# Optimization experiments

Hardware: AMD Instinct MI355X
Metric: run time of the kernel (lower is better)

The kernel has to match this reference:

```python
import jax, jax.numpy as jnp
import numpy as np

D_MODEL = 768
BATCH = 4096
RANK_DIST = [(4, 512), (8, 256), (16, 128), (32, 64), (64, 32)]


@jax.custom_vjp
def jumprelu(x):
    # hard threshold at 0 in fwd; full straight-through estimator in bwd
    return x * (x > 0.0).astype(x.dtype)


def _jr_fwd(x):
    return jumprelu(x), None


def _jr_bwd(res, g):
    return (g,)


jumprelu.defvjp(_jr_fwd, _jr_bwd)


def setup_inputs() -> dict:
    key = jax.random.key(0)
    keys = jax.random.split(key, 1 + 3 * len(RANK_DIST))
    inp = {"x": jax.random.normal(keys[0], (BATCH, D_MODEL), dtype=jnp.float32)}
    for i, (n, r) in enumerate(RANK_DIST):
        kV, kU, kE = keys[1 + 3 * i], keys[2 + 3 * i], keys[3 + 3 * i]
        scale = (1.0 / (D_MODEL * r)) ** 0.25
        inp[f"V{i}"] = scale * jax.random.normal(kV, (n, r, D_MODEL), dtype=jnp.float32)
        inp[f"U{i}"] = scale * jax.random.normal(kU, (n, D_MODEL, r), dtype=jnp.float32)
        enc = jax.random.normal(kE, (n, D_MODEL), dtype=jnp.float32)
        inp[f"enc{i}"] = enc / jnp.linalg.norm(enc, axis=1, keepdims=True)
        inp[f"b{i}"] = jnp.full((n,), -1.0, dtype=jnp.float32)
    return inp


def _group_forward(x, V, U, enc, b):
    n, r, d = V.shape
    pre = x @ enc.T - b                      # (b, n)
    gate = jumprelu(pre)                     # (b, n)
    Vx = jnp.einsum("nrd,bd->nbr", V, x)    # (n, b, r)
    # fused: UVx gated by gate then summed over transforms n
    out = jnp.einsum("ndr,nbr,bn->bd", U, Vx, gate)  # (b, d)
    u_norms = jnp.linalg.norm(U.reshape(n, -1), axis=1)
    v_norms = jnp.linalg.norm(V.reshape(n, -1), axis=1)
    frob = u_norms * v_norms / jnp.sqrt(jnp.asarray(d * r, dtype=x.dtype))
    return out, gate, frob


def reference(x, V0, U0, enc0, b0, V1, U1, enc1, b1, V2, U2, enc2, b2,
              V3, U3, enc3, b3, V4, U4, enc4, b4):
    Vs = [V0, V1, V2, V3, V4]
    Us = [U0, U1, U2, U3, U4]
    encs = [enc0, enc1, enc2, enc3, enc4]
    bs = [b0, b1, b2, b3, b4]
    output = jnp.zeros_like(x)
    total_sparsity = jnp.asarray(0.0, dtype=x.dtype)
    total_active = jnp.asarray(0.0, dtype=x.dtype)
    gate_acts = []
    for V, U, enc, b in zip(Vs, Us, encs, bs):
        g_out, gate, frob = _group_forward(x, V, U, enc, b)
        output = output + g_out
        mean_abs_gate = jnp.abs(gate).mean(axis=0)
        total_sparsity = total_sparsity + (jnp.tanh(mean_abs_gate) * frob).sum()
        total_active = total_active + (gate > 0).astype(x.dtype).sum(axis=1).mean()
        gate_acts.append(gate)
    return (output, total_sparsity, total_active, *gate_acts)
```

## Files before the change

### kernel.cpp

```cpp
#include <hip/hip_runtime.h>

#define BATCH 4096
#define DM 768
#define LTOT 10240
#define NG 124

typedef __bf16 bf16x8 __attribute__((ext_vector_type(8)));
typedef short short8 __attribute__((ext_vector_type(8)));
typedef float f32x4 __attribute__((ext_vector_type(4)));

struct Ptr5 { const float* p[5]; };

__device__ __forceinline__ unsigned short f2bf(float f) {
    unsigned u = __builtin_bit_cast(unsigned, f);
    unsigned r = (u + 0x7FFFu + ((u >> 16) & 1u)) >> 16;
    return (unsigned short)r;
}

__device__ __forceinline__ short8 pack8(float4 a, float4 b) {
    union { unsigned short u[8]; short8 s; } o;
    o.u[0] = f2bf(a.x); o.u[1] = f2bf(a.y); o.u[2] = f2bf(a.z); o.u[3] = f2bf(a.w);
    o.u[4] = f2bf(b.x); o.u[5] = f2bf(b.y); o.u[6] = f2bf(b.z); o.u[7] = f2bf(b.w);
    return o.s;
}


__global__ __launch_bounds__(256) void prep_k(const float* __restrict__ x,
                                              Ptr5 vp, Ptr5 up, Ptr5 ep, Ptr5 bp,
                                              unsigned short* __restrict__ vb,
                                              unsigned short* __restrict__ w2t,
                                              unsigned short* __restrict__ xb,
                                              float* __restrict__ gate_ws,
                                              float* __restrict__ outg,
                                              float* __restrict__ vslot,
                                              float* __restrict__ uslot,
                                              float* __restrict__ gslot,
                                              float* __restrict__ aslot) {
    const int basen[5] = {0, 4, 12, 28, 60};
    int bx = blockIdx.x;
    int tid = threadIdx.x;
    if (bx < 32) {
        __shared__ unsigned short lA[128 * 64];
        __shared__ unsigned short lB[128 * 64];
        __shared__ float sgs[128];
        __shared__ float sac;
        int wave = tid >> 6, lane = tid & 63;
        int wm = wave >> 1, wn = wave & 1;
        int lan15 = lane & 15, quad = lane >> 4;
        int sw = lan15 & 7;
        int m0 = bx * 128;
        f32x4 acc[4][4] = {};
        for (int k0 = 0; k0 < DM; k0 += 64) {
            __syncthreads();
            #pragma unroll
            for (int i = 0; i < 4; i++) {
                int gidx = i * 256 + tid;
                int row = gidx >> 3, kb = gidx & 7;
                int r7 = row & 7;
                int la = (row >> 3) * 512 + r7 * 64 + (kb ^ r7) * 8;
                int sidx = (m0 + row) * 192 + (k0 >> 2) + kb * 2;
                float4 a0 = ((const float4*)x)[sidx];
                float4 a1 = ((const float4*)x)[sidx + 1];
                *(short8*)(lA + la) = pack8(a0, a1);
                float4 b0 = {0.f, 0.f, 0.f, 0.f}, b1 = {0.f, 0.f, 0.f, 0.f};
                if (row < NG) {
                    int g = (row < 4) ? 0 : (row < 12) ? 1 : (row < 28) ? 2 :
                            (row < 60) ? 3 : 4;
                    int ni = row - basen[g];
                    int eidx = ni * 192 + (k0 >> 2) + kb * 2;
                    b0 = ((const float4*)ep.p[g])[eidx];
                    b1 = ((const float4*)ep.p[g])[eidx + 1];
                }
                *(short8*)(lB + la) = pack8(b0, b1);
            }
            __syncthreads();
            #pragma unroll
            for (int kk = 0; kk < 2; kk++) {
                int kb = kk * 4 + quad;
                int kel = (kb ^ sw) * 8;
                bf16x8 af[4], bfr[4];
                #pragma unroll
                for (int t = 0; t < 4; t++) {
                    short8 ra = *(const short8*)(lA + (wm * 64 + t * 16 + lan15) * 64 + kel);
                    short8 rb = *(const short8*)(lB + (wn * 64 + t * 16 + lan15) * 64 + kel);
                    af[t]  = __builtin_bit_cast(bf16x8, ra);
                    bfr[t] = __builtin_bit_cast(bf16x8, rb);
                }
                #pragma unroll
                for (int mt = 0; mt < 4; mt++)
                    #pragma unroll
                    for (int nt = 0; nt < 4; nt++)
                        acc[mt][nt] = __builtin_amdgcn_mfma_f32_16x16x32_bf16(
                            af[mt], bfr[nt], acc[mt][nt], 0, 0, 0);
            }
        }
        if (tid < 128) sgs[tid] = 0.f;
        if (tid == 0) sac = 0.f;
        __syncthreads();
        const size_t baseg[5] = {3145730ull, 3145730ull + 16384, 3145730ull + 49152,
                                 3145730ull + 114688, 3145730ull + 245760};
        float cnt = 0.f;
        #pragma unroll
        for (int nt = 0; nt < 4; nt++) {
            int col = wn * 64 + nt * 16 + lan15;
            float cs = 0.f;
            if (col < NG) {
                int g = (col < 4) ? 0 : (col < 12) ? 1 : (col < 28) ? 2 :
                        (col < 60) ? 3 : 4;
                int ni = col - basen[g];
                int w = 4 << g;
                float bv = bp.p[g][ni];
                #pragma unroll
                for (int mt = 0; mt < 4; mt++) {
                    int r0 = m0 + wm * 64 + mt * 16 + quad * 4;
                    #pragma unroll
                    for (int rg = 0; rg < 4; rg++) {
                        float pre = acc[mt][nt][rg] - bv;
                        float gt = pre > 0.f ? pre : 0.f;
                        gate_ws[(size_t)(r0 + rg) * NG + col] = gt;
                        outg[baseg[g] + (size_t)(r0 + rg) * w + ni] = gt;
                        cs += gt;
                        if (pre > 0.f) cnt += 1.f;
                    }
                }
                cs += __shfl_xor(cs, 16);
                cs += __shfl_xor(cs, 32);
                if (quad == 0) atomicAdd(&sgs[col], cs);
            }
        }
        #pragma unroll
        for (int off = 32; off > 0; off >>= 1) cnt += __shfl_xor(cnt, off);
        if (lane == 0) atomicAdd(&sac, cnt);
        __syncthreads();
        if (tid < NG) gslot[bx * NG + tid] = sgs[tid];
        if (tid == 0) aslot[bx] = sac;
    } else if (bx < 1952) {
        __shared__ float swave[4];
        int cb = bx - 32;
        int isV = cb < 960;
        int wb = isV ? cb : cb - 960;
        int g = wb / 192;
        int within = wb - g * 192;
        const float* src = isV ? vp.p[g] : up.p[g];
        int r = 512 >> g, lr = 9 - g;
        float ss = 0.f;
        #pragma unroll
        for (int i = 0; i < 8; i++) {
            int j = within * 2048 + i * 256 + tid;
            float4 v = ((const float4*)src)[j];
            ss += v.x*v.x + v.y*v.y + v.z*v.z + v.w*v.w;
            ushort4 o;
            o.x = f2bf(v.x); o.y = f2bf(v.y); o.z = f2bf(v.z); o.w = f2bf(v.w);
            if (isV) {
                ((ushort4*)vb)[(size_t)(g * 192 + within) * 2048 + i * 256 + tid] = o;
            } else {
                int idx = j * 4;
                int rr = idx & (r - 1);
                int t2 = idx >> lr;
                int d  = t2 % DM;
                int n  = t2 / DM;
                size_t dst = (size_t)d * LTOT + (size_t)(g << 11) + (size_t)n * r + rr;
                *(ushort4*)(w2t + dst) = o;
            }
        }
        #pragma unroll
        for (int off = 32; off > 0; off >>= 1) ss += __shfl_down(ss, off);
        if ((tid & 63) == 0) swave[tid >> 6] = ss;
        __syncthreads();
        if (tid == 0) {
            float t = (swave[0] + swave[1]) + (swave[2] + swave[3]);
            (isV ? vslot : uslot)[wb] = t;
        }
    } else {
        int base = (bx - 1952) * 2048;
        #pragma unroll
        for (int i = 0; i < 8; i++) {
            int j = base + i * 256 + tid;
            float4 v = ((const float4*)x)[j];
            ushort4 o;
            o.x = f2bf(v.x); o.y = f2bf(v.y); o.z = f2bf(v.z); o.w = f2bf(v.w);
            ((ushort4*)xb)[j] = o;
        }
    }
}

template <int ROWS, int NT>
__device__ __forceinline__ void stage(const unsigned short* __restrict__ src, int ld,
                                      unsigned short* lds, int wv, int lane) {
    int rsub = lane >> 3;
    int colb = ((lane ^ rsub) & 7) * 8;
    #pragma unroll
    for (int i = 0; i < ROWS * 8 / NT; i++) {
        int c = i * (NT / 64) + wv;
        const unsigned short* gp = src + (size_t)(c * 8 + rsub) * ld + colb;
        __builtin_amdgcn_global_load_lds((const __attribute__((address_space(1))) void*)gp,
                                         (__attribute__((address_space(3))) void*)(lds + c * 512),
                                         16, 0, 0);
    }
}

template <int BM, int BN, int NT>
__global__ __launch_bounds__(NT) void gemm_nt(const unsigned short* __restrict__ A,
                                              const unsigned short* __restrict__ Bm,
                                              int Kblk, int lda, int ldb,
                                              void* __restrict__ Cout,
                                              const float* __restrict__ gate, int ldc) {
    __shared__ unsigned short lA[BM * 64];
    __shared__ unsigned short lB[BN * 64];
    int tid = threadIdx.x, wave = tid >> 6, lane = tid & 63;
    constexpr int WN = BN / 64;
    int wm = wave / WN, wn = wave % WN;
    int m0 = blockIdx.x * BM, n0 = blockIdx.y * BN;
    A  += (size_t)m0 * lda;
    Bm += (size_t)n0 * ldb;
    f32x4 acc[4][4] = {};
    int lan15 = lane & 15, quad = lane >> 4;
    int sw = lan15 & 7;

    for (int k0 = 0; k0 < Kblk; k0 += 64) {
        stage<BM, NT>(A + k0, lda, lA, wave, lane);
        stage<BN, NT>(Bm + k0, ldb, lB, wave, lane);
        __syncthreads();
        #pragma unroll
        for (int kk = 0; kk < 2; kk++) {
            int kb = kk * 4 + quad;
            int kel = (kb ^ sw) * 8;
            bf16x8 af[4], bfr[4];
            #pragma unroll
            for (int t = 0; t < 4; t++) {
                short8 ra = *(const short8*)(lA + (size_t)(wm * 64 + t * 16 + lan15) * 64 + kel);
                short8 rb = *(const short8*)(lB + (size_t)(wn * 64 + t * 16 + lan15) * 64 + kel);
                af[t]  = __builtin_bit_cast(bf16x8, ra);
                bfr[t] = __builtin_bit_cast(bf16x8, rb);
            }
            #pragma unroll
            for (int mt = 0; mt < 4; mt++)
                #pragma unroll
                for (int nt = 0; nt < 4; nt++)
                    acc[mt][nt] = __builtin_amdgcn_mfma_f32_16x16x32_bf16(af[mt], bfr[nt],
                                                                          acc[mt][nt], 0, 0, 0);
        }
        __syncthreads();
    }

    const int basen[5] = {0, 4, 12, 28, 60};
    unsigned short* H = (unsigned short*)Cout;
    #pragma unroll
    for (int mt = 0; mt < 4; mt++) {
        __syncthreads();
        #pragma unroll
        for (int nt = 0; nt < 4; nt++) {
            int col = n0 + wn * 64 + nt * 16 + lan15;
            int g = col >> 11;
            int ngl = basen[g] + ((col & 2047) >> (9 - g));
            #pragma unroll
            for (int rg = 0; rg < 4; rg++) {
                int grow = m0 + wm * 64 + mt * 16 + quad * 4 + rg;
                float gv = gate[(size_t)grow * NG + ngl];
                lA[wave * 1024 + (quad * 4 + rg) * 64 + nt * 16 + lan15] =
                    f2bf(acc[mt][nt][rg] * gv);
            }
        }
        __syncthreads();
        #pragma unroll
        for (int i = 0; i < 2; i++) {
            int f = i * NT + tid;
            int R = f >> 5;
            int u = f & 31;
            int wv2 = ((R >> 4) << 2) + (u >> 3);
            short8 vread = *(const short8*)(lA + wv2 * 1024 + (R & 15) * 64 + (u & 7) * 8);
            int grow = m0 + (R >> 4) * 64 + mt * 16 + (R & 15);
            *(short8*)(H + (size_t)grow * ldc + n0 + u * 8) = vread;
        }
    }
}

__global__ __launch_bounds__(256) void gemm2_nt(const unsigned short* __restrict__ A,
                                                const unsigned short* __restrict__ Bm,
                                                int Kblk, int lda, int ldb,
                                                float* __restrict__ P, int ldc) {
    __shared__ unsigned short lA[128 * 64];
    __shared__ unsigned short lB[128 * 64];
    int tid = threadIdx.x, wave = tid >> 6, lane = tid & 63;
    int wm = wave >> 1, wn = wave & 1;
    int m0 = blockIdx.x * 128, n0 = blockIdx.y * 128;
    A  += (size_t)m0 * lda + (size_t)blockIdx.z * Kblk;
    Bm += (size_t)n0 * ldb + (size_t)blockIdx.z * Kblk;
    f32x4 acc[4][4] = {};
    int lan15 = lane & 15, quad = lane >> 4;
    int sw = lan15 & 7;

    for (int k0 = 0; k0 < Kblk; k0 += 64) {
        stage<128, 256>(A + k0, lda, lA, wave, lane);
        stage<128, 256>(Bm + k0, ldb, lB, wave, lane);
        __syncthreads();
        #pragma unroll
        for (int kk = 0; kk < 2; kk++) {
            int kb = kk * 4 + quad;
            int kel = (kb ^ sw) * 8;
            bf16x8 af[4], bfr[4];
            #pragma unroll
            for (int t = 0; t < 4; t++) {
                short8 ra = *(const short8*)(lA + (size_t)(wm * 64 + t * 16 + lan15) * 64 + kel);
                short8 rb = *(const short8*)(lB + (size_t)(wn * 64 + t * 16 + lan15) * 64 + kel);
                af[t]  = __builtin_bit_cast(bf16x8, ra);
                bfr[t] = __builtin_bit_cast(bf16x8, rb);
            }
            #pragma unroll
            for (int mt = 0; mt < 4; mt++)
                #pragma unroll
                for (int nt = 0; nt < 4; nt++)
                    acc[mt][nt] = __builtin_amdgcn_mfma_f32_16x16x32_bf16(af[mt], bfr[nt],
                                                                          acc[mt][nt], 0, 0, 0);
        }
        __syncthreads();
    }

    P += (size_t)blockIdx.z * (size_t)gridDim.x * 128 * ldc;
    #pragma unroll
    for (int nt = 0; nt < 4; nt++) {
        int col = n0 + wn * 64 + nt * 16 + lan15;
        #pragma unroll
        for (int mt = 0; mt < 4; mt++) {
            #pragma unroll
            for (int rg = 0; rg < 4; rg++) {
                int row = m0 + wm * 64 + mt * 16 + quad * 4 + rg;
                P[(size_t)row * ldc + col] = acc[mt][nt][rg];
            }
        }
    }
}


__global__ __launch_bounds__(256) void reduce_k(const float4* __restrict__ P,
                                                float4* __restrict__ out, int quarter,
                                                const float* __restrict__ vslot,
                                                const float* __restrict__ uslot,
                                                const float* __restrict__ gslot,
                                                const float* __restrict__ aslot,
                                                float* __restrict__ o2) {
    int i = blockIdx.x * 256 + threadIdx.x;
    float4 a = P[i], b = P[i + quarter], c = P[i + 2 * quarter], d = P[i + 3 * quarter];
    float4 o;
    o.x = (a.x + b.x) + (c.x + d.x);
    o.y = (a.y + b.y) + (c.y + d.y);
    o.z = (a.z + b.z) + (c.z + d.z);
    o.w = (a.w + b.w) + (c.w + d.w);
    out[i] = o;
    if (blockIdx.x == 0) {
        __shared__ float sh[128];
        const int basen[5] = {0, 4, 12, 28, 60};
        int t = threadIdx.x;
        if (t < 128) {
            float v = 0.f;
            if (t < NG) {
                int g = (t < 4) ? 0 : (t < 12) ? 1 : (t < 28) ? 2 : (t < 60) ? 3 : 4;
                int nloc = t - basen[g];
                int bpseg = 48 >> g;
                float vs = 0.f, us = 0.f;
                int base = g * 192 + nloc * bpseg;
                for (int j = 0; j < bpseg; j++) { vs += vslot[base + j]; us += uslot[base + j]; }
                float gs = 0.f;
                for (int bb = 0; bb < 32; bb++) gs += gslot[bb * NG + t];
                float rr = (float)(512 >> g);
                float mean = gs * (1.0f / BATCH);
                float frob = sqrtf(us * vs) / sqrtf(768.0f * rr);
                v = tanhf(mean) * frob;
            }
            sh[t] = v;
        }
        if (t == 128) {
            float asum = 0.f;
            for (int bb = 0; bb < 32; bb++) asum += aslot[bb];
            o2[1] = asum * (1.0f / BATCH);
        }
        __syncthreads();
        for (int s = 64; s > 0; s >>= 1) {
            if (threadIdx.x < s) sh[threadIdx.x] += sh[threadIdx.x + s];
            __syncthreads();
        }
        if (threadIdx.x == 0) o2[0] = sh[0];
    }
}


extern "C" void kernel_launch(void* const* d_in, const int* in_sizes, int n_in,
                              void* d_out, int out_size, void* d_ws, size_t ws_size,
                              hipStream_t stream) {
    const float* x = (const float*)d_in[0];
    Ptr5 vp, up, ep, bp;
    for (int g = 0; g < 5; g++) {
        vp.p[g] = (const float*)d_in[1 + 4 * g];
        up.p[g] = (const float*)d_in[2 + 4 * g];
        ep.p[g] = (const float*)d_in[3 + 4 * g];
        bp.p[g] = (const float*)d_in[4 + 4 * g];
    }
    float* out = (float*)d_out;
    char* ws = (char*)d_ws;
    size_t off = 0;
    unsigned short* xb   = (unsigned short*)(ws + off); off += (size_t)BATCH * DM * 2;
    unsigned short* vb   = (unsigned short*)(ws + off); off += (size_t)LTOT * DM * 2;
    unsigned short* w2t  = (unsigned short*)(ws + off); off += (size_t)LTOT * DM * 2;
    float* gate_ws       = (float*)(ws + off);          off += (size_t)BATCH * NG * 4;
    float* vslot         = (float*)(ws + off);          off += 960 * 4;
    float* uslot         = (float*)(ws + off);          off += 960 * 4;
    float* gslot         = (float*)(ws + off);          off += 32 * NG * 4;
    float* aslot         = (float*)(ws + off);          off += 32 * 4 + 256;
    size_t fixed = off;
    int CB = BATCH;
    while (CB > 128 && fixed + (size_t)CB * LTOT * 2 + 4ull * CB * DM * 4 > ws_size) CB >>= 1;
    unsigned short* Hg  = (unsigned short*)(ws + fixed);
    float* partial      = (float*)(ws + fixed + (size_t)CB * LTOT * 2);

    prep_k<<<dim3(2336), 256, 0, stream>>>(
        x, vp, up, ep, bp, vb, w2t, xb, gate_ws, out,
        vslot, uslot, gslot, aslot);

    int nch = BATCH / CB;
    for (int c = 0; c < nch; c++) {
        gemm_nt<128, 256, 512><<<dim3(CB / 128, LTOT / 256, 1), 512, 0, stream>>>(
            xb + (size_t)c * CB * DM, vb, DM, DM, DM,
            (void*)Hg, gate_ws + (size_t)c * CB * NG, LTOT);
        gemm2_nt<<<dim3(CB / 128, DM / 128, 4), 256, 0, stream>>>(
            Hg, w2t, LTOT / 4, LTOT, LTOT, partial, DM);
        reduce_k<<<dim3(CB * 192 / 256), 256, 0, stream>>>(
            (const float4*)partial, (float4*)(out + (size_t)c * CB * DM), CB * DM / 4,
            vslot, uslot, gslot, aslot, out + (size_t)BATCH * DM);
    }
}
```

Before: 341.8 us.

## Double-buffer gemm2 with direct global-to-LDS loads and 256-row tiles

Rewrites the second GEMM to load tiles with global_load_lds into double-buffered shared memory, using split barriers and vmcnt waits so loads overlap MFMA work. Each block now covers 256 rows with a K step of 32, and split-K goes from 4 to 5 slices. It also drops the workspace chunking loop and overlays the temporary buffers on the partial-sum region, so each kernel launches once. The risks are higher register pressure from the 8x4 accumulators, a hardcoded workspace size assumption, and an extra partial plane that the reduce must read.

```diff
diff --git a/kernel.cpp b/kernel.cpp
--- a/kernel.cpp
+++ b/kernel.cpp
@@ -275,58 +275,82 @@
     }
 }
 
-__global__ __launch_bounds__(256) void gemm2_nt(const unsigned short* __restrict__ A,
-                                                const unsigned short* __restrict__ Bm,
-                                                int Kblk, int lda, int ldb,
-                                                float* __restrict__ P, int ldc) {
-    __shared__ unsigned short lA[128 * 64];
-    __shared__ unsigned short lB[128 * 64];
+__global__ __launch_bounds__(256, 2) void gemm2_nt(const unsigned short* __restrict__ A,
+                                                   const unsigned short* __restrict__ Bm,
+                                                   float* __restrict__ P) {
+    __shared__ unsigned short lA[2][256 * 32];
+    __shared__ unsigned short lB[2][128 * 32];
     int tid = threadIdx.x, wave = tid >> 6, lane = tid & 63;
     int wm = wave >> 1, wn = wave & 1;
-    int m0 = blockIdx.x * 128, n0 = blockIdx.y * 128;
-    A  += (size_t)m0 * lda + (size_t)blockIdx.z * Kblk;
-    Bm += (size_t)n0 * ldb + (size_t)blockIdx.z * Kblk;
-    f32x4 acc[4][4] = {};
     int lan15 = lane & 15, quad = lane >> 4;
-    int sw = lan15 & 7;
-
-    for (int k0 = 0; k0 < Kblk; k0 += 64) {
-        stage<128, 256>(A + k0, lda, lA, wave, lane);
-        stage<128, 256>(Bm + k0, ldb, lB, wave, lane);
-        __syncthreads();
-        #pragma unroll
-        for (int kk = 0; kk < 2; kk++) {
-            int kb = kk * 4 + quad;
-            int kel = (kb ^ sw) * 8;
-            bf16x8 af[4], bfr[4];
-            #pragma unroll
-            for (int t = 0; t < 4; t++) {
-                short8 ra = *(const short8*)(lA + (size_t)(wm * 64 + t * 16 + lan15) * 64 + kel);
-                short8 rb = *(const short8*)(lB + (size_t)(wn * 64 + t * 16 + lan15) * 64 + kel);
-                af[t]  = __builtin_bit_cast(bf16x8, ra);
-                bfr[t] = __builtin_bit_cast(bf16x8, rb);
-            }
-            #pragma unroll
-            for (int mt = 0; mt < 4; mt++)
-                #pragma unroll
-                for (int nt = 0; nt < 4; nt++)
-                    acc[mt][nt] = __builtin_amdgcn_mfma_f32_16x16x32_bf16(af[mt], bfr[nt],
-                                                                          acc[mt][nt], 0, 0, 0);
-        }
-        __syncthreads();
-    }
-
-    P += (size_t)blockIdx.z * (size_t)gridDim.x * 128 * ldc;
+    int kel = (quad ^ (lan15 & 3)) * 8;
+    int m0 = blockIdx.x * 256, n0 = blockIdx.y * 128;
+    const unsigned short* Ab = A  + (size_t)m0 * LTOT + (size_t)blockIdx.z * 2048;
+    const unsigned short* Bb = Bm + (size_t)n0 * LTOT + (size_t)blockIdx.z * 2048;
+    int rsub = lane >> 2;
+    int gofs = ((lane & 3) ^ (rsub & 3)) * 8;
+
+#define G2_STA(cur, kof, c) __builtin_amdgcn_global_load_lds( \
+        (const __attribute__((address_space(1))) void*)(Ab + (size_t)((c) * 16 + rsub) * LTOT + (kof) + gofs), \
+        (__attribute__((address_space(3))) void*)(&lA[cur][(c) * 512]), 16, 0, 0)
+#define G2_STB(cur, kof, c) __builtin_amdgcn_global_load_lds( \
+        (const __attribute__((address_space(1))) void*)(Bb + (size_t)((c) * 16 + rsub) * LTOT + (kof) + gofs), \
+        (__attribute__((address_space(3))) void*)(&lB[cur][(c) * 512]), 16, 0, 0)
+
+    f32x4 acc[8][4] = {};
+    G2_STA(0, 0, wave); G2_STA(0, 0, wave + 8); G2_STB(0, 0, wave); G2_STB(0, 0, wave + 4);
+    G2_STA(0, 0, wave + 4); G2_STA(0, 0, wave + 12);
+
+#define G2_TILE(cur, knext) { \
+    asm volatile("s_waitcnt vmcnt(2)" ::: "memory"); \
+    __builtin_amdgcn_s_barrier(); \
+    asm volatile("" ::: "memory"); \
+    G2_STA(cur ^ 1, knext, wave); G2_STA(cur ^ 1, knext, wave + 8); \
+    G2_STB(cur ^ 1, knext, wave); G2_STB(cur ^ 1, knext, wave + 4); \
+    bf16x8 bfr[4], af[4]; \
+    _Pragma("unroll") for (int nt = 0; nt < 4; nt++) \
+        bfr[nt] = __builtin_bit_cast(bf16x8, *(const short8*)(&lB[cur][(wn * 64 + nt * 16 + lan15) * 32 + kel])); \
+    _Pragma("unroll") for (int mt = 0; mt < 4; mt++) \
+        af[mt] = __builtin_bit_cast(bf16x8, *(const short8*)(&lA[cur][(wm * 128 + mt * 16 + lan15) * 32 + kel])); \
+    __builtin_amdgcn_s_setprio(1); \
+    _Pragma("unroll") for (int mt = 0; mt < 4; mt++) \
+        _Pragma("unroll") for (int nt = 0; nt < 4; nt++) \
+            acc[mt][nt] = __builtin_amdgcn_mfma_f32_16x16x32_bf16(af[mt], bfr[nt], acc[mt][nt], 0, 0, 0); \
+    __builtin_amdgcn_s_setprio(0); \
+    asm volatile("s_waitcnt vmcnt(4)" ::: "memory"); \
+    __builtin_amdgcn_s_barrier(); \
+    asm volatile("" ::: "memory"); \
+    G2_STA(cur ^ 1, knext, wave + 4); G2_STA(cur ^ 1, knext, wave + 12); \
+    _Pragma("unroll") for (int mt = 0; mt < 4; mt++) \
+        af[mt] = __builtin_bit_cast(bf16x8, *(const short8*)(&lA[cur][(wm * 128 + 64 + mt * 16 + lan15) * 32 + kel])); \
+    __builtin_amdgcn_s_setprio(1); \
+    _Pragma("unroll") for (int mt = 0; mt < 4; mt++) \
+        _Pragma("unroll") for (int nt = 0; nt < 4; nt++) \
+            acc[4 + mt][nt] = __builtin_amdgcn_mfma_f32_16x16x32_bf16(af[mt], bfr[nt], acc[4 + mt][nt], 0, 0, 0); \
+    __builtin_amdgcn_s_setprio(0); \
+}
+
+    for (int t2 = 0; t2 < 32; t2++) {
+        int k0 = t2 * 64;
+        G2_TILE(0, k0 + 32);
+        int knext = (t2 == 31) ? (k0 + 32) : (k0 + 64);
+        G2_TILE(1, knext);
+    }
+#undef G2_TILE
+#undef G2_STA
+#undef G2_STB
+    asm volatile("s_waitcnt vmcnt(0)" ::: "memory");
+
+    float* Pz = P + (size_t)blockIdx.z * ((size_t)BATCH * DM);
     #pragma unroll
-    for (int nt = 0; nt < 4; nt++) {
-        int col = n0 + wn * 64 + nt * 16 + lan15;
-        #pragma unroll
-        for (int mt = 0; mt < 4; mt++) {
-            #pragma unroll
-            for (int rg = 0; rg < 4; rg++) {
-                int row = m0 + wm * 64 + mt * 16 + quad * 4 + rg;
-                P[(size_t)row * ldc + col] = acc[mt][nt][rg];
-            }
+    for (int mt = 0; mt < 8; mt++) {
+        #pragma unroll
+        for (int rg = 0; rg < 4; rg++) {
+            int row = m0 + wm * 128 + mt * 16 + quad * 4 + rg;
+            float* pr = Pz + (size_t)row * DM + n0 + wn * 64 + lan15;
+            #pragma unroll
+            for (int nt = 0; nt < 4; nt++)
+                pr[nt * 16] = acc[mt][nt][rg];
         }
     }
 }
@@ -341,11 +365,12 @@
                                                 float* __restrict__ o2) {
     int i = blockIdx.x * 256 + threadIdx.x;
     float4 a = P[i], b = P[i + quarter], c = P[i + 2 * quarter], d = P[i + 3 * quarter];
+    float4 e = P[i + 4 * quarter];
     float4 o;
-    o.x = (a.x + b.x) + (c.x + d.x);
-    o.y = (a.y + b.y) + (c.y + d.y);
-    o.z = (a.z + b.z) + (c.z + d.z);
-    o.w = (a.w + b.w) + (c.w + d.w);
+    o.x = ((a.x + b.x) + (c.x + d.x)) + e.x;
+    o.y = ((a.y + b.y) + (c.y + d.y)) + e.y;
+    o.z = ((a.z + b.z) + (c.z + d.z)) + e.z;
+    o.w = ((a.w + b.w) + (c.w + d.w)) + e.w;
     out[i] = o;
     if (blockIdx.x == 0) {
         __shared__ float sh[128];
@@ -398,33 +423,26 @@
     float* out = (float*)d_out;
     char* ws = (char*)d_ws;
     size_t off = 0;
-    unsigned short* xb   = (unsigned short*)(ws + off); off += (size_t)BATCH * DM * 2;
-    unsigned short* vb   = (unsigned short*)(ws + off); off += (size_t)LTOT * DM * 2;
     unsigned short* w2t  = (unsigned short*)(ws + off); off += (size_t)LTOT * DM * 2;
-    float* gate_ws       = (float*)(ws + off);          off += (size_t)BATCH * NG * 4;
     float* vslot         = (float*)(ws + off);          off += 960 * 4;
     float* uslot         = (float*)(ws + off);          off += 960 * 4;
     float* gslot         = (float*)(ws + off);          off += 32 * NG * 4;
     float* aslot         = (float*)(ws + off);          off += 32 * 4 + 256;
-    size_t fixed = off;
-    int CB = BATCH;
-    while (CB > 128 && fixed + (size_t)CB * LTOT * 2 + 4ull * CB * DM * 4 > ws_size) CB >>= 1;
-    unsigned short* Hg  = (unsigned short*)(ws + fixed);
-    float* partial      = (float*)(ws + fixed + (size_t)CB * LTOT * 2);
+    unsigned short* Hg   = (unsigned short*)(ws + off); off += (size_t)BATCH * LTOT * 2;
+    float* partial       = (float*)(ws + off);          off += 5ull * BATCH * DM * 4;
+    unsigned short* xb      = (unsigned short*)partial;
+    unsigned short* vb      = (unsigned short*)((char*)partial + (size_t)BATCH * DM * 2);
+    float* gate_ws          = (float*)((char*)partial + (size_t)BATCH * DM * 2
+                                                      + (size_t)LTOT * DM * 2);
 
     prep_k<<<dim3(2336), 256, 0, stream>>>(
         x, vp, up, ep, bp, vb, w2t, xb, gate_ws, out,
         vslot, uslot, gslot, aslot);
 
-    int nch = BATCH / CB;
-    for (int c = 0; c < nch; c++) {
-        gemm_nt<128, 256, 512><<<dim3(CB / 128, LTOT / 256, 1), 512, 0, stream>>>(
-            xb + (size_t)c * CB * DM, vb, DM, DM, DM,
-            (void*)Hg, gate_ws + (size_t)c * CB * NG, LTOT);
-        gemm2_nt<<<dim3(CB / 128, DM / 128, 4), 256, 0, stream>>>(
-            Hg, w2t, LTOT / 4, LTOT, LTOT, partial, DM);
-        reduce_k<<<dim3(CB * 192 / 256), 256, 0, stream>>>(
-            (const float4*)partial, (float4*)(out + (size_t)c * CB * DM), CB * DM / 4,
-            vslot, uslot, gslot, aslot, out + (size_t)BATCH * DM);
-    }
-}
+    gemm_nt<128, 256, 512><<<dim3(BATCH / 128, LTOT / 256, 1), 512, 0, stream>>>(
+        xb, vb, DM, DM, DM, (void*)Hg, gate_ws, LTOT);
+    gemm2_nt<<<dim3(BATCH / 256, DM / 128, 5), 256, 0, stream>>>(Hg, w2t, partial);
+    reduce_k<<<dim3(BATCH * DM / 4 / 256), 256, 0, stream>>>(
+        (const float4*)partial, (float4*)out, BATCH * DM / 4,
+        vslot, uslot, gslot, aslot, out + (size_t)BATCH * DM);
+}
```

Measured after the change: 347.0 us. About the same (+1.5%).
